# Performance work log

Measured on AMD Instinct MI355X. Metric: run time of the kernel, lower is better.

The kernel has to match this reference:

```python
import jax, jax.numpy as jnp
import numpy as np

# Semantics of GPTQ Marlin 2:4 int4 GEMM: W_dense[K,N] has exactly 2 nonzeros per
# group of 4 along K. Compressed int4 values (q-8)*scale are stored packed 8-per-int32
# in B [K/16, N]; meta [K/4, N] in [0,6) selects which pair of the 4 positions is
# nonzero (index into the 6 combinations). s [K/groupsize, N] are group scales.

_PAIRS = jnp.array([[0, 1], [0, 2], [0, 3], [1, 2], [1, 3], [2, 3]], dtype=jnp.int32)


def _dequant_24(B, meta, s):
    Kd16, N = B.shape
    K = Kd16 * 16
    # unpack 8 nibbles per int32 -> [K/2, N] compressed values
    shifts = (jnp.arange(8, dtype=jnp.int32) * 4)[None, :, None]
    nib = (B[:, None, :] >> shifts) & 0xF            # [K/16, 8, N]
    vals = nib.reshape(K // 2, N).astype(jnp.float32) - 8.0  # symmetric zero-point 8
    gs = K // s.shape[0]                              # original groupsize
    scale = jnp.repeat(s, gs // 2, axis=0)            # [K/2, N] (compressed K dim)
    deq = (vals * scale).reshape(K // 4, 2, N)        # 2 values per group of 4
    pos = _PAIRS[meta]                                # [K/4, N, 2] positions in [0,4)
    oh = jax.nn.one_hot(pos, 4, dtype=jnp.float32)    # [K/4, N, 2, 4]
    W = jnp.einsum('gjn,gnjp->gpn', deq, oh)          # scatter into group slots
    return W.reshape(K, N)


def setup_inputs() -> dict:
    key = jax.random.key(0)
    k0, k1, k2, k3, k4 = jax.random.split(key, 5)
    M, K, N, GS = 8192, 4096, 4096, 128
    A = jax.random.normal(k0, (M, K), dtype=jnp.float32)
    B = jax.random.randint(k1, (K // 16, N), 0, 2147483647, dtype=jnp.int32)
    meta = jax.random.randint(k2, (K // 4, N), 0, 6, dtype=jnp.int32)
    s = jax.random.uniform(k3, (K // GS, N), dtype=jnp.float32, minval=0.005, maxval=0.02)
    bias = jax.random.normal(k4, (N,), dtype=jnp.float32)
    return {"A": A, "B": B, "meta": meta, "s": s, "bias": bias}


def reference(A, B, meta, s, bias):
    W = _dequant_24(B, meta, s)          # [K, N] dense 2:4-sparse dequantized weight
    return jnp.matmul(A, W, preferred_element_type=jnp.float32) + bias
```

## Files before the change

kernel.cpp:

```cpp
#include <hip/hip_runtime.h>

typedef _Float16 h16;
typedef __attribute__((ext_vector_type(8))) _Float16 h16x8;
typedef __attribute__((ext_vector_type(4))) float f32x4;
typedef unsigned int u32;

#define BARRIER() __builtin_amdgcn_s_barrier()
#define SCHEDB()  __builtin_amdgcn_sched_barrier(0)

__global__ __launch_bounds__(256) void cvtA_kernel(const float* __restrict__ A,
                                                   h16* __restrict__ Ah, int total8) {
  int stride = gridDim.x * blockDim.x;
  for (int i = blockIdx.x * blockDim.x + threadIdx.x; i < total8; i += stride) {
    const f32x4* p = (const f32x4*)(A + (size_t)i * 8);
    f32x4 v0 = p[0], v1 = p[1];
    h16x8 o;
    o[0] = (h16)v0[0]; o[1] = (h16)v0[1]; o[2] = (h16)v0[2]; o[3] = (h16)v0[3];
    o[4] = (h16)v1[0]; o[5] = (h16)v1[1]; o[6] = (h16)v1[2]; o[7] = (h16)v1[3];
    *(h16x8*)(Ah + (size_t)i * 8) = o;
  }
}

__global__ __launch_bounds__(256) void dequant_kernel(const int* __restrict__ Bq,
    const int* __restrict__ meta, const float* __restrict__ s,
    h16* __restrict__ Wt, int K, int N, int chunksPerGroup) {
  int n = blockIdx.x * 256 + threadIdx.x;
  int chunk = blockIdx.y;
  u32 w0 = (u32)Bq[(size_t)(chunk * 2) * N + n];
  u32 w1 = (u32)Bq[(size_t)(chunk * 2 + 1) * N + n];
  float sc = s[(size_t)(chunk / chunksPerGroup) * N + n];
  h16 out[32];
#pragma unroll
  for (int gi = 0; gi < 8; ++gi) {
    int g = chunk * 8 + gi;
    int mm = meta[(size_t)g * N + n];
    u32 w = (gi < 4) ? w0 : w1;
    int j0 = (2 * gi) & 7;
    float d0 = (float)((int)((w >> (4 * j0)) & 0xFu) - 8) * sc;
    float d1 = (float)((int)((w >> (4 * j0 + 4)) & 0xFu) - 8) * sc;
    u32 enc = (0xED9C84u >> (4 * mm)) & 0xFu;
    int p0 = (int)(enc & 3u), p1 = (int)(enc >> 2);
#pragma unroll
    for (int p = 0; p < 4; ++p) {
      float v = (p == p0) ? d0 : ((p == p1) ? d1 : 0.0f);
      out[gi * 4 + p] = (h16)v;
    }
  }
  h16* dst = Wt + (size_t)n * K + chunk * 32;
  *(h16x8*)(dst + 0)  = *(h16x8*)(out + 0);
  *(h16x8*)(dst + 8)  = *(h16x8*)(out + 8);
  *(h16x8*)(dst + 16) = *(h16x8*)(out + 16);
  *(h16x8*)(dst + 24) = *(h16x8*)(out + 24);
}

__global__ __launch_bounds__(512, 2) void gemm_kernel(const h16* __restrict__ A,
    const h16* __restrict__ Wt, const float* __restrict__ bias,
    float* __restrict__ C, int M, int N, int K) {
  __shared__ alignas(16) h16 As[2 * 2 * 8192];
  __shared__ alignas(16) h16 Bs[2 * 2 * 8192];

  const int nTilesN = N >> 8;
  const int nwg = gridDim.x;
  int bid = blockIdx.x;
  int wg = (bid & 7) * (nwg >> 3) + (bid >> 3);
  int tm = wg / nTilesN, tn = wg - tm * nTilesN;

  const int tid = threadIdx.x;
  const int lane = tid & 63, w = tid >> 6;
  const int wr = w >> 2, wc = w & 3;

  const int i0 = tid >> 3;
  const int sigma = (tid & 7) ^ ((tid >> 3) & 7);
  const h16* gA_t = A + ((size_t)(tm * 256) + i0) * K + sigma * 8;
  const int rB0 = ((i0 >> 5) << 6) + (i0 & 31);
  const h16* gB_t = Wt + ((size_t)(tn * 256) + rB0) * K + sigma * 8;
  const int tid8 = tid * 8;
  const size_t rowK128 = (size_t)128 * K;

#define GLOAD(SRC, DST) __builtin_amdgcn_global_load_lds(                      \
    (const __attribute__((address_space(1))) void*)(SRC),                      \
    (__attribute__((address_space(3))) void*)(DST), 16, 0, 0)

#define STAGE_A(T_, mh_) do {                                                  \
    const h16* s_ = gA_t + (size_t)((mh_) * 64) * K + (T_) * 64;               \
    h16* d_ = As + ((((T_) & 1) * 2 + (mh_)) * 8192) + tid8;                   \
    GLOAD(s_, d_); GLOAD(s_ + rowK128, d_ + 4096); } while (0)

#define STAGE_B(T_, nh_) do {                                                  \
    const h16* s_ = gB_t + (size_t)((nh_) * 32) * K + (T_) * 64;               \
    h16* d_ = Bs + ((((T_) & 1) * 2 + (nh_)) * 8192) + tid8;                   \
    GLOAD(s_, d_); GLOAD(s_ + rowK128, d_ + 4096); } while (0)

  const int ln15 = lane & 15, l16 = lane >> 4, l7 = lane & 7;
  const int aRow = (wr * 64 + ln15) * 64;
  const int bRow = (wc * 32 + ln15) * 64;
  const int sl0 = ((0 + l16) ^ l7) * 8;
  const int sl1 = ((4 + l16) ^ l7) * 8;

  f32x4 acc[8][4] = {};
  const int NT = K >> 6;

  STAGE_A(0, 0); STAGE_B(0, 0); STAGE_B(0, 1); STAGE_A(0, 1);
  STAGE_A(1, 0); STAGE_B(1, 0); STAGE_B(1, 1);
  asm volatile("s_waitcnt vmcnt(6)" ::: "memory");
  SCHEDB();
  BARRIER();

  for (int T = 0; T < NT; ++T) {
    const int buf = T & 1;
    const h16* a0 = As + (buf * 2 + 0) * 8192;
    const h16* a1 = As + (buf * 2 + 1) * 8192;
    const h16* b0 = Bs + (buf * 2 + 0) * 8192;
    const h16* b1 = Bs + (buf * 2 + 1) * 8192;
    h16x8 af[4][2], bf0[2][2], bf1[2][2];

#pragma unroll
    for (int n = 0; n < 2; ++n) {
      bf0[n][0] = *(const h16x8*)(b0 + bRow + n * 1024 + sl0);
      bf0[n][1] = *(const h16x8*)(b0 + bRow + n * 1024 + sl1);
    }
#pragma unroll
    for (int m = 0; m < 4; ++m) {
      af[m][0] = *(const h16x8*)(a0 + aRow + m * 1024 + sl0);
      af[m][1] = *(const h16x8*)(a0 + aRow + m * 1024 + sl1);
    }
    if (T + 1 < NT) STAGE_A(T + 1, 1);
    SCHEDB();
    BARRIER();
    __builtin_amdgcn_s_setprio(1);
#pragma unroll
    for (int m = 0; m < 4; ++m)
#pragma unroll
      for (int n = 0; n < 2; ++n) {
        acc[m][n] = __builtin_amdgcn_mfma_f32_16x16x32_f16(af[m][0], bf0[n][0], acc[m][n], 0, 0, 0);
        acc[m][n] = __builtin_amdgcn_mfma_f32_16x16x32_f16(af[m][1], bf0[n][1], acc[m][n], 0, 0, 0);
      }
    __builtin_amdgcn_s_setprio(0);
    SCHEDB();
    BARRIER();

#pragma unroll
    for (int n = 0; n < 2; ++n) {
      bf1[n][0] = *(const h16x8*)(b1 + bRow + n * 1024 + sl0);
      bf1[n][1] = *(const h16x8*)(b1 + bRow + n * 1024 + sl1);
    }
    if (T + 2 < NT) STAGE_A(T + 2, 0);
    SCHEDB();
    BARRIER();
    __builtin_amdgcn_s_setprio(1);
#pragma unroll
    for (int m = 0; m < 4; ++m)
#pragma unroll
      for (int n = 0; n < 2; ++n) {
        acc[m][2 + n] = __builtin_amdgcn_mfma_f32_16x16x32_f16(af[m][0], bf1[n][0], acc[m][2 + n], 0, 0, 0);
        acc[m][2 + n] = __builtin_amdgcn_mfma_f32_16x16x32_f16(af[m][1], bf1[n][1], acc[m][2 + n], 0, 0, 0);
      }
    __builtin_amdgcn_s_setprio(0);
    SCHEDB();
    BARRIER();

#pragma unroll
    for (int m = 0; m < 4; ++m) {
      af[m][0] = *(const h16x8*)(a1 + aRow + m * 1024 + sl0);
      af[m][1] = *(const h16x8*)(a1 + aRow + m * 1024 + sl1);
    }
    if (T + 2 < NT) STAGE_B(T + 2, 0);
    SCHEDB();
    BARRIER();
    __builtin_amdgcn_s_setprio(1);
#pragma unroll
    for (int m = 0; m < 4; ++m)
#pragma unroll
      for (int n = 0; n < 2; ++n) {
        acc[4 + m][2 + n] = __builtin_amdgcn_mfma_f32_16x16x32_f16(af[m][0], bf1[n][0], acc[4 + m][2 + n], 0, 0, 0);
        acc[4 + m][2 + n] = __builtin_amdgcn_mfma_f32_16x16x32_f16(af[m][1], bf1[n][1], acc[4 + m][2 + n], 0, 0, 0);
      }
    __builtin_amdgcn_s_setprio(0);
    SCHEDB();
    BARRIER();

    if (T + 2 < NT) STAGE_B(T + 2, 1);
    SCHEDB();
    BARRIER();
    __builtin_amdgcn_s_setprio(1);
#pragma unroll
    for (int m = 0; m < 4; ++m)
#pragma unroll
      for (int n = 0; n < 2; ++n) {
        acc[4 + m][n] = __builtin_amdgcn_mfma_f32_16x16x32_f16(af[m][0], bf0[n][0], acc[4 + m][n], 0, 0, 0);
        acc[4 + m][n] = __builtin_amdgcn_mfma_f32_16x16x32_f16(af[m][1], bf0[n][1], acc[4 + m][n], 0, 0, 0);
      }
    __builtin_amdgcn_s_setprio(0);
    if (T < NT - 2) {
      asm volatile("s_waitcnt vmcnt(6)" ::: "memory");
    } else if (T == NT - 2) {
      asm volatile("s_waitcnt vmcnt(0)" ::: "memory");
    }
    SCHEDB();
    BARRIER();
  }

  int colBase = tn * 256 + wc * 64 + ln15;
  int rowBase = tm * 256 + wr * 128 + l16 * 4;
#pragma unroll
  for (int n = 0; n < 4; ++n) {
    float bv = bias[colBase + n * 16];
#pragma unroll
    for (int m = 0; m < 8; ++m) {
#pragma unroll
      for (int j = 0; j < 4; ++j) {
        C[(size_t)(rowBase + m * 16 + j) * N + colBase + n * 16] = acc[m][n][j] + bv;
      }
    }
  }
#undef STAGE_A
#undef STAGE_B
#undef GLOAD
}

extern "C" void kernel_launch(void* const* d_in, const int* in_sizes, int n_in,
                              void* d_out, int out_size, void* d_ws, size_t ws_size,
                              hipStream_t stream) {
  const float* A = (const float*)d_in[0];
  const int* Bq = (const int*)d_in[1];
  const int* meta = (const int*)d_in[2];
  const float* s = (const float*)d_in[3];
  const float* bias = (const float*)d_in[4];
  float* C = (float*)d_out;

  const int N = in_sizes[4];
  const int K = (int)(((long long)in_sizes[1] * 16) / N);
  const int M = (int)((long long)in_sizes[0] / K);
  const int sRows = (int)((long long)in_sizes[3] / N);
  const int chunksPerGroup = (K / sRows) / 32;

  h16* Ah = (h16*)d_ws;
  h16* Wt = Ah + (size_t)M * K;

  cvtA_kernel<<<2048, 256, 0, stream>>>(A, Ah, (M * K) / 8);

  dim3 dgrid(N / 256, K / 32);
  dequant_kernel<<<dgrid, 256, 0, stream>>>(Bq, meta, s, Wt, K, N, chunksPerGroup);

  int grid = (M / 256) * (N / 256);
  gemm_kernel<<<grid, 512, 0, stream>>>(Ah, Wt, bias, C, M, N, K);
}
```

Before: 304.1 us.

## Unroll GEMM main loop by two and use finer-grained vmcnt waits with B-fragment prefetch

Restructures the GEMM K-loop into a 2x unrolled macro with static LDS buffer pointers. B fragments for the next tile are read ahead into a ping-pong register set. Each phase now uses its own s_waitcnt vmcnt so it waits only for the global->LDS loads it depends on, instead of one coarse wait per tile. The aim is to hide more load latency and remove per-iteration address arithmetic. The price is extra register pressure from the additional B fragment set, and hand-tuned vmcnt values that must match the exact load ordering.

```diff
diff --git a/kernel.cpp b/kernel.cpp
--- a/kernel.cpp
+++ b/kernel.cpp
@@ -7,6 +7,8 @@
 
 #define BARRIER() __builtin_amdgcn_s_barrier()
 #define SCHEDB()  __builtin_amdgcn_sched_barrier(0)
+#define VMCNT_(n) asm volatile("s_waitcnt vmcnt(" #n ")" ::: "memory")
+#define VMCNT(n)  VMCNT_(n)
 
 __global__ __launch_bounds__(256) void cvtA_kernel(const float* __restrict__ A,
                                                    h16* __restrict__ Ah, int total8) {
@@ -53,6 +55,33 @@
   *(h16x8*)(dst + 24) = *(h16x8*)(out + 24);
 }
 
+__device__ __forceinline__ void rd4(h16x8 (&d)[4][2], const h16* base, int row,
+                                    int s0, int s1) {
+#pragma unroll
+  for (int m = 0; m < 4; ++m) {
+    d[m][0] = *(const h16x8*)(base + row + m * 1024 + s0);
+    d[m][1] = *(const h16x8*)(base + row + m * 1024 + s1);
+  }
+}
+__device__ __forceinline__ void rd2(h16x8 (&d)[2][2], const h16* base, int row,
+                                    int s0, int s1) {
+#pragma unroll
+  for (int n = 0; n < 2; ++n) {
+    d[n][0] = *(const h16x8*)(base + row + n * 1024 + s0);
+    d[n][1] = *(const h16x8*)(base + row + n * 1024 + s1);
+  }
+}
+__device__ __forceinline__ void mmaQ(f32x4 (&acc)[8][4], int mo, int no,
+                                     const h16x8 (&a)[4][2], const h16x8 (&b)[2][2]) {
+#pragma unroll
+  for (int m = 0; m < 4; ++m)
+#pragma unroll
+    for (int n = 0; n < 2; ++n) {
+      acc[mo + m][no + n] = __builtin_amdgcn_mfma_f32_16x16x32_f16(a[m][0], b[n][0], acc[mo + m][no + n], 0, 0, 0);
+      acc[mo + m][no + n] = __builtin_amdgcn_mfma_f32_16x16x32_f16(a[m][1], b[n][1], acc[mo + m][no + n], 0, 0, 0);
+    }
+}
+
 __global__ __launch_bounds__(512, 2) void gemm_kernel(const h16* __restrict__ A,
     const h16* __restrict__ Wt, const float* __restrict__ bias,
     float* __restrict__ C, int M, int N, int K) {
@@ -98,106 +127,59 @@
   const int sl1 = ((4 + l16) ^ l7) * 8;
 
   f32x4 acc[8][4] = {};
+  h16x8 afA[4][2], bX[2][2], bY[2][2];
   const int NT = K >> 6;
+  const int NTh = NT >> 1;
 
   STAGE_A(0, 0); STAGE_B(0, 0); STAGE_B(0, 1); STAGE_A(0, 1);
   STAGE_A(1, 0); STAGE_B(1, 0); STAGE_B(1, 1);
-  asm volatile("s_waitcnt vmcnt(6)" ::: "memory");
+  VMCNT(10);
+  BARRIER();
+  rd2(bX, Bs, bRow, sl0, sl1);
   SCHEDB();
+  VMCNT(8);
   BARRIER();
 
-  for (int T = 0; T < NT; ++T) {
-    const int buf = T & 1;
-    const h16* a0 = As + (buf * 2 + 0) * 8192;
-    const h16* a1 = As + (buf * 2 + 1) * 8192;
-    const h16* b0 = Bs + (buf * 2 + 0) * 8192;
-    const h16* b1 = Bs + (buf * 2 + 1) * 8192;
-    h16x8 af[4][2], bf0[2][2], bf1[2][2];
-
-#pragma unroll
-    for (int n = 0; n < 2; ++n) {
-      bf0[n][0] = *(const h16x8*)(b0 + bRow + n * 1024 + sl0);
-      bf0[n][1] = *(const h16x8*)(b0 + bRow + n * 1024 + sl1);
-    }
-#pragma unroll
-    for (int m = 0; m < 4; ++m) {
-      af[m][0] = *(const h16x8*)(a0 + aRow + m * 1024 + sl0);
-      af[m][1] = *(const h16x8*)(a0 + aRow + m * 1024 + sl1);
-    }
-    if (T + 1 < NT) STAGE_A(T + 1, 1);
-    SCHEDB();
-    BARRIER();
-    __builtin_amdgcn_s_setprio(1);
-#pragma unroll
-    for (int m = 0; m < 4; ++m)
-#pragma unroll
-      for (int n = 0; n < 2; ++n) {
-        acc[m][n] = __builtin_amdgcn_mfma_f32_16x16x32_f16(af[m][0], bf0[n][0], acc[m][n], 0, 0, 0);
-        acc[m][n] = __builtin_amdgcn_mfma_f32_16x16x32_f16(af[m][1], bf0[n][1], acc[m][n], 0, 0, 0);
-      }
-    __builtin_amdgcn_s_setprio(0);
-    SCHEDB();
-    BARRIER();
-
-#pragma unroll
-    for (int n = 0; n < 2; ++n) {
-      bf1[n][0] = *(const h16x8*)(b1 + bRow + n * 1024 + sl0);
-      bf1[n][1] = *(const h16x8*)(b1 + bRow + n * 1024 + sl1);
-    }
-    if (T + 2 < NT) STAGE_A(T + 2, 0);
-    SCHEDB();
-    BARRIER();
-    __builtin_amdgcn_s_setprio(1);
-#pragma unroll
-    for (int m = 0; m < 4; ++m)
-#pragma unroll
-      for (int n = 0; n < 2; ++n) {
-        acc[m][2 + n] = __builtin_amdgcn_mfma_f32_16x16x32_f16(af[m][0], bf1[n][0], acc[m][2 + n], 0, 0, 0);
-        acc[m][2 + n] = __builtin_amdgcn_mfma_f32_16x16x32_f16(af[m][1], bf1[n][1], acc[m][2 + n], 0, 0, 0);
-      }
-    __builtin_amdgcn_s_setprio(0);
-    SCHEDB();
-    BARRIER();
-
-#pragma unroll
-    for (int m = 0; m < 4; ++m) {
-      af[m][0] = *(const h16x8*)(a1 + aRow + m * 1024 + sl0);
-      af[m][1] = *(const h16x8*)(a1 + aRow + m * 1024 + sl1);
-    }
-    if (T + 2 < NT) STAGE_B(T + 2, 0);
-    SCHEDB();
-    BARRIER();
-    __builtin_amdgcn_s_setprio(1);
-#pragma unroll
-    for (int m = 0; m < 4; ++m)
-#pragma unroll
-      for (int n = 0; n < 2; ++n) {
-        acc[4 + m][2 + n] = __builtin_amdgcn_mfma_f32_16x16x32_f16(af[m][0], bf1[n][0], acc[4 + m][2 + n], 0, 0, 0);
-        acc[4 + m][2 + n] = __builtin_amdgcn_mfma_f32_16x16x32_f16(af[m][1], bf1[n][1], acc[4 + m][2 + n], 0, 0, 0);
-      }
-    __builtin_amdgcn_s_setprio(0);
-    SCHEDB();
-    BARRIER();
-
-    if (T + 2 < NT) STAGE_B(T + 2, 1);
-    SCHEDB();
-    BARRIER();
-    __builtin_amdgcn_s_setprio(1);
-#pragma unroll
-    for (int m = 0; m < 4; ++m)
-#pragma unroll
-      for (int n = 0; n < 2; ++n) {
-        acc[4 + m][n] = __builtin_amdgcn_mfma_f32_16x16x32_f16(af[m][0], bf0[n][0], acc[4 + m][n], 0, 0, 0);
-        acc[4 + m][n] = __builtin_amdgcn_mfma_f32_16x16x32_f16(af[m][1], bf0[n][1], acc[4 + m][n], 0, 0, 0);
-      }
-    __builtin_amdgcn_s_setprio(0);
-    if (T < NT - 2) {
-      asm volatile("s_waitcnt vmcnt(6)" ::: "memory");
-    } else if (T == NT - 2) {
-      asm volatile("s_waitcnt vmcnt(0)" ::: "memory");
-    }
-    SCHEDB();
-    BARRIER();
+#define TILE(T_, A0_, A1_, B1_, B0n_, H0_, H1_, G1_, G_, GR_, V1_, V2_, V3_, V4_) do { \
+                                                             \
+    rd4(afA, A0_, aRow, sl0, sl1);                                \
+    rd2(H1_, B1_, bRow, sl0, sl1);                                \
+    if (G1_) STAGE_A((T_) + 1, 1);                                             \
+    SCHEDB(); VMCNT(V1_); BARRIER();                                           \
+    __builtin_amdgcn_s_setprio(1); mmaQ(acc, 0, 0, afA, H0_);                  \
+    __builtin_amdgcn_s_setprio(0); SCHEDB(); BARRIER();                        \
+                                                             \
+    if (G_) STAGE_A((T_) + 2, 0);                                              \
+    SCHEDB(); VMCNT(V2_); BARRIER();                                           \
+    __builtin_amdgcn_s_setprio(1); mmaQ(acc, 0, 2, afA, H1_);                  \
+    __builtin_amdgcn_s_setprio(0); SCHEDB(); BARRIER();                        \
+                                                             \
+    rd4(afA, A1_, aRow, sl0, sl1);                                \
+    if (G_) STAGE_B((T_) + 2, 0);                                              \
+    SCHEDB(); VMCNT(V3_); BARRIER();                                           \
+    __builtin_amdgcn_s_setprio(1); mmaQ(acc, 4, 2, afA, H1_);                  \
+    __builtin_amdgcn_s_setprio(0); SCHEDB(); BARRIER();                        \
+                                                             \
+    if (GR_) rd2(H1_, B0n_, bRow, sl0, sl1);          \
+    if (G_) STAGE_B((T_) + 2, 1);                                              \
+    SCHEDB(); VMCNT(V4_); BARRIER();                                           \
+    __builtin_amdgcn_s_setprio(1); mmaQ(acc, 4, 0, afA, H0_);                  \
+    __builtin_amdgcn_s_setprio(0); SCHEDB(); BARRIER();                        \
+  } while (0)
+
+  for (int it = 0; it < NTh - 1; ++it) {
+    const int T = it * 2;
+    TILE(T,     As,         As + 8192,  Bs + 8192,  Bs + 16384, bX, bY,
+         true, true, true, 8, 8, 8, 8);
+    TILE(T + 1, As + 16384, As + 24576, Bs + 24576, Bs,         bY, bX,
+         true, true, true, 8, 8, 8, 8);
+  }
+  {
+    const int T = NT - 2;
+    TILE(T,     As,         As + 8192,  Bs + 8192,  Bs + 16384, bX, bY,
+         true,  false, true,  8, 8, 4, 2);
+    TILE(T + 1, As + 16384, As + 24576, Bs + 24576, Bs,         bY, bX,
+         false, false, false, 0, 0, 0, 0);
   }
 
   int colBase = tn * 256 + wc * 64 + ln15;
@@ -213,6 +195,7 @@
       }
     }
   }
+#undef TILE
 #undef STAGE_A
 #undef STAGE_B
 #undef GLOAD
```

Measured after the change: 324.5 us. 1.07x slower.
